# Kernel tuning notes

Measured on AMD Instinct MI355X. Metric: run time of the kernel, lower is better.

The kernel has to match this reference:

```python
import jax, jax.numpy as jnp
import numpy as np

E = 2048      # embed_dim
HQ = 16       # query heads
HK = 4        # kv heads
D = E // HQ   # head_dim = 128
G = HQ // HK  # head groups = 4
KVE = D * HK  # kv_embed_dim = 512
B, N = 2, 2048


def setup_inputs() -> dict:
    key = jax.random.key(0)
    ks = jax.random.split(key, 8)
    s_q = (2.0 / (E + E)) ** 0.5      # xavier_normal for square proj
    s_kv = (2.0 / (E + KVE)) ** 0.5   # xavier_normal for kv proj
    return {
        "query": jax.random.normal(ks[0], (B, N, E), jnp.float32),
        "key":   jax.random.normal(ks[1], (B, N, E), jnp.float32),
        "value": jax.random.normal(ks[2], (B, N, E), jnp.float32),
        "Wq": jax.random.normal(ks[3], (E, E), jnp.float32) * s_q,
        "bq_": jnp.zeros((E,), jnp.float32),
        "Wk": jax.random.normal(ks[4], (KVE, E), jnp.float32) * s_kv,
        "bk_": jnp.zeros((KVE,), jnp.float32),
        "Wv": jax.random.normal(ks[5], (KVE, E), jnp.float32) * s_kv,
        "bv_": jnp.zeros((KVE,), jnp.float32),
        "Wo": jax.random.normal(ks[6], (E, E), jnp.float32) * s_q,
        "bo_": jnp.zeros((E,), jnp.float32),
        "is_causal": 1,
    }


def reference(query, key, value, Wq, bq_, Wk, bk_, Wv, bv_, Wo, bo_, is_causal):
    b, n, _ = query.shape
    s = key.shape[1]
    # projections (torch Linear: y = x @ W.T + b)
    q = (query @ Wq.T + bq_).reshape(b, n, HQ, D).transpose(0, 2, 1, 3)  # b hq n d
    k = (key   @ Wk.T + bk_).reshape(b, s, HK, D).transpose(0, 2, 1, 3)  # b hk s d
    v = (value @ Wv.T + bv_).reshape(b, s, HK, D).transpose(0, 2, 1, 3)  # b hk s d
    q = q / (D ** 0.5)
    # split query heads 'b (h g) n d -> b g h n d' (h = kv heads outer, g inner)
    qg = q.reshape(b, HK, G, n, D).transpose(0, 2, 1, 3, 4)              # b g h n d
    sim = jnp.einsum('bghnd,bhsd->bghns', qg, k)                          # b g h n s
    if is_causal:
        causal = jnp.tril(jnp.ones((n, s), dtype=bool))
        sim = jnp.where(causal, sim, jnp.finfo(sim.dtype).min)
    attn = jax.nn.softmax(sim, axis=-1)
    out = jnp.einsum('bghns,bhsd->bghnd', attn, v)                        # b g h n d
    # 'b g h n d -> b n (h g) d' then merge heads
    out = out.transpose(0, 3, 2, 1, 4).reshape(b, n, E)
    return out @ Wo.T + bo_
```

## Files before the change

### kernel.cpp

```cpp
#include <hip/hip_runtime.h>
#include <stdint.h>

#define E_   2048
#define HQ_  16
#define HK_  4
#define D_   128
#define G_   4
#define KVE_ 512
#define B_   2
#define N_   2048
#define MTOT (B_*N_)

#define QSC 0.12751743f

typedef __attribute__((ext_vector_type(8))) short bf16x8;
typedef __attribute__((ext_vector_type(4))) float f32x4;

__device__ __forceinline__ unsigned short f2bf(float f) {
  union { float f; uint32_t u; } a; a.f = f;
  uint32_t u = a.u;
  uint32_t r = (u + 0x7fffu + ((u >> 16) & 1u)) >> 16;
  return (unsigned short)r;
}

__device__ __forceinline__ uint32_t pack_bf2(float a, float b) {
  union { float f; uint32_t u; } x, y; x.f = a; y.f = b;
  return (x.u >> 16) | (y.u & 0xffff0000u);
}

__device__ __forceinline__ void g2l16(const void* g, void* l) {
  __builtin_amdgcn_global_load_lds(
      (__attribute__((address_space(1))) void*)(void*)(uintptr_t)g,
      (__attribute__((address_space(3))) void*)l,
      16, 0, 0);
}

__global__ void cast_all(const float* __restrict__ q, const float* __restrict__ k,
                         const float* __restrict__ v, const float* __restrict__ wq,
                         const float* __restrict__ wk, const float* __restrict__ wv,
                         const float* __restrict__ wo, unsigned short* __restrict__ dst) {
  int i = blockIdx.x * 256 + threadIdx.x;
  const float* src; int base;
  if      (i < 2097152) { src = q;  base = 0; }
  else if (i < 4194304) { src = k;  base = 2097152; }
  else if (i < 6291456) { src = v;  base = 4194304; }
  else if (i < 7340032) { src = wq; base = 6291456; }
  else if (i < 7602176) { src = wk; base = 7340032; }
  else if (i < 7864320) { src = wv; base = 7602176; }
  else                  { src = wo; base = 7864320; }
  float4 val = ((const float4*)src)[i - base];
  ushort4 o;
  o.x = f2bf(val.x); o.y = f2bf(val.y); o.z = f2bf(val.z); o.w = f2bf(val.w);
  ((ushort4*)dst)[i] = o;
}

__device__ __forceinline__ void gemm_kloop(const unsigned short* __restrict__ A,
                                           const unsigned short* __restrict__ W,
                                           unsigned short* As, unsigned short* Bs,
                                           int bm, int bn, int K,
                                           int wm, int wn, int tid, int l16, int quad,
                                           f32x4 acc[4][4]) {
  for (int k0 = 0; k0 < K; k0 += 32) {
    __syncthreads();
#pragma unroll
    for (int r = 0; r < 2; ++r) {
      int c = r * 256 + tid;
      int row = c >> 2, c8 = (c & 3) << 3;
      g2l16(A + (size_t)(bm + row) * K + k0 + c8, (char*)As + (size_t)c * 16);
    }
#pragma unroll
    for (int r = 0; r < 2; ++r) {
      int c = r * 256 + tid;
      int row = c >> 2, c8 = (c & 3) << 3;
      g2l16(W + (size_t)(bn + row) * K + k0 + c8, (char*)Bs + (size_t)c * 16);
    }
    __syncthreads();

    bf16x8 af[4], bf[4];
#pragma unroll
    for (int mi = 0; mi < 4; ++mi)
      af[mi] = *(const bf16x8*)(As + (wm + mi * 16 + l16) * 32 + quad * 8);
#pragma unroll
    for (int ni = 0; ni < 4; ++ni)
      bf[ni] = *(const bf16x8*)(Bs + (wn + ni * 16 + l16) * 32 + quad * 8);
#pragma unroll
    for (int mi = 0; mi < 4; ++mi)
#pragma unroll
      for (int ni = 0; ni < 4; ++ni)
        acc[mi][ni] = __builtin_amdgcn_mfma_f32_16x16x32_bf16(af[mi], bf[ni], acc[mi][ni], 0, 0, 0);
  }
}

__global__ __launch_bounds__(256, 3)
void proj_fused(const unsigned short* __restrict__ qb, const unsigned short* __restrict__ kb,
                const unsigned short* __restrict__ vb,
                const unsigned short* __restrict__ Wqb, const unsigned short* __restrict__ Wkb,
                const unsigned short* __restrict__ Wvb,
                const float* __restrict__ bq, const float* __restrict__ bk,
                const float* __restrict__ bv,
                unsigned short* __restrict__ Qb, unsigned short* __restrict__ Kpp,
                unsigned short* __restrict__ Vtt) {
  __shared__ unsigned short As[128 * 32];
  __shared__ unsigned short Bs[128 * 32];
  const int tid  = threadIdx.x;
  const int wave = tid >> 6, lane = tid & 63;
  const int l16  = lane & 15, quad = lane >> 4;
  const int bm = blockIdx.x * 128;
  const int wm = (wave & 1) * 64, wn = (wave >> 1) * 64;
  const int y = blockIdx.y;

  const unsigned short *A, *W;
  const float* bias;
  unsigned short* out;
  int bn, mode, Nn;
  float scale;
  if (y < 16)      { A = qb; W = Wqb; bias = bq; out = Qb;  bn = y * 128;        mode = 0; Nn = 2048; scale = QSC;  }
  else if (y < 20) { A = kb; W = Wkb; bias = bk; out = Kpp; bn = (y - 16) * 128; mode = 0; Nn = 512;  scale = 1.0f; }
  else             { A = vb; W = Wvb; bias = bv; out = Vtt; bn = (y - 20) * 128; mode = 1; Nn = 512;  scale = 1.0f; }

  f32x4 acc[4][4] = {};
  gemm_kloop(A, W, As, Bs, bm, bn, E_, wm, wn, tid, l16, quad, acc);

  if (mode == 0) {
#pragma unroll
    for (int mi = 0; mi < 4; ++mi)
#pragma unroll
      for (int ni = 0; ni < 4; ++ni) {
        int col = bn + wn + ni * 16 + l16;
        float bb = bias[col];
        int row0 = bm + wm + mi * 16 + quad * 4;
#pragma unroll
        for (int r = 0; r < 4; ++r)
          out[(size_t)(row0 + r) * Nn + col] = f2bf((acc[mi][ni][r] + bb) * scale);
      }
  } else {
#pragma unroll
    for (int mi = 0; mi < 4; ++mi)
#pragma unroll
      for (int ni = 0; ni < 4; ++ni) {
        int col = bn + wn + ni * 16 + l16;
        float bb = bias[col];
        int row0 = bm + wm + mi * 16 + quad * 4;
        int b = row0 >> 11, s = row0 & 2047;
        ushort4 o;
        o.x = f2bf(acc[mi][ni][0] + bb);
        o.y = f2bf(acc[mi][ni][1] + bb);
        o.z = f2bf(acc[mi][ni][2] + bb);
        o.w = f2bf(acc[mi][ni][3] + bb);
        *(ushort4*)(out + (size_t)(b * KVE_ + col) * N_ + s) = o;
      }
  }
}

__global__ __launch_bounds__(256, 2)
void gemm_out(const unsigned short* __restrict__ A, const unsigned short* __restrict__ W,
              const float* __restrict__ bias, float* __restrict__ Cout) {
  __shared__ unsigned short As[128 * 32];
  __shared__ unsigned short Bs[128 * 32];
  const int tid  = threadIdx.x;
  const int wave = tid >> 6, lane = tid & 63;
  const int l16  = lane & 15, quad = lane >> 4;
  const int bm = blockIdx.x * 128, bn = blockIdx.y * 128;
  const int wm = (wave & 1) * 64, wn = (wave >> 1) * 64;

  f32x4 acc[4][4] = {};
  gemm_kloop(A, W, As, Bs, bm, bn, E_, wm, wn, tid, l16, quad, acc);

#pragma unroll
  for (int mi = 0; mi < 4; ++mi)
#pragma unroll
    for (int ni = 0; ni < 4; ++ni) {
      int col = bn + wn + ni * 16 + l16;
      float bb = bias[col];
      int row0 = bm + wm + mi * 16 + quad * 4;
#pragma unroll
      for (int r = 0; r < 4; ++r)
        Cout[(size_t)(row0 + r) * E_ + col] = acc[mi][ni][r] + bb;
    }
}

__global__ __launch_bounds__(256, 3)
void attn_gqa(const unsigned short* __restrict__ Qp,
              const unsigned short* __restrict__ Kp,
              const unsigned short* __restrict__ Vt,
              unsigned short* __restrict__ Ob,
              const int* __restrict__ is_causal_p) {
  __shared__ unsigned short lds[2][8192];
  __shared__ float Xt[256];

  const int tid  = threadIdx.x;
  const int wave = tid >> 6, lane = tid & 63;
  const int l16  = lane & 15, quad = lane >> 4;
  const int qg = wave >> 1, sg = wave & 1;
  const int bh = blockIdx.y;
  const int u  = (blockIdx.x + bh) & 31;
  const int qt = (u < 16) ? u : 47 - u;
  const int b = bh >> 4, hq = bh & 15, hk = hq >> 2;
  const int causal = *is_causal_p;

  const unsigned short* Kbase = Kp + (size_t)b * N_ * KVE_ + hk * D_;
  const unsigned short* Vbase = Vt + (size_t)(b * KVE_ + hk * D_) * N_;

  const int nt = causal ? qt + 1 : (N_ / 64);
  const int qw = qt * 64 + qg * 32;

  auto stage = [&](int t, int buf) {
    int s0 = t * 64;
    unsigned short* Kd = &lds[buf][0];
#pragma unroll
    for (int r = 0; r < 4; ++r) {
      int idx = r * 256 + tid;
      int s = (idx >> 8) * 16 + (idx & 15);
      int d = ((idx >> 6) & 3) * 32 + ((idx >> 4) & 3) * 8;
      g2l16(Kbase + (size_t)(s0 + s) * KVE_ + d, Kd + (size_t)idx * 8);
    }
  };

  bf16x8 qf[2][4];
#pragma unroll
  for (int mi = 0; mi < 2; ++mi)
#pragma unroll
    for (int kk = 0; kk < 4; ++kk)
      qf[mi][kk] = *(const bf16x8*)(Qp + (size_t)(b * N_ + qw + mi * 16 + l16) * E_ +
                                    hq * D_ + kk * 32 + quad * 8);

  f32x4 o[2][8] = {};
  float tsum[2] = { 0.f, 0.f };

  stage(0, 0);
  __syncthreads();

  for (int t = 0; t < nt; ++t) {
    if (t + 1 < nt) stage(t + 1, (t + 1) & 1);
    const unsigned short* Kb = &lds[t & 1][0];
    const int sw = t * 64 + sg * 32;
    const bool active = !causal || (sw <= qw + 31);

    if (active) {
      f32x4 sa[2][2] = {};
#pragma unroll
      for (int kk = 0; kk < 4; ++kk) {
        bf16x8 kf[2];
#pragma unroll
        for (int ni = 0; ni < 2; ++ni)
          kf[ni] = *(const bf16x8*)(Kb + (((sg * 2 + ni) * 4 + kk) * 64 + lane) * 8);
#pragma unroll
        for (int mi = 0; mi < 2; ++mi)
#pragma unroll
          for (int ni = 0; ni < 2; ++ni)
            sa[mi][ni] = __builtin_amdgcn_mfma_f32_16x16x32_bf16(kf[ni], qf[mi][kk], sa[mi][ni], 0, 0, 0);
      }

      bf16x8 vf[8];
#pragma unroll
      for (int n8 = 0; n8 < 8; ++n8)
        vf[n8] = *(const bf16x8*)(Vbase + (size_t)(n8 * 16 + l16) * N_ + sw + quad * 8);

      if (causal && sw + 31 > qw) {
#pragma unroll
        for (int mi = 0; mi < 2; ++mi)
#pragma unroll
          for (int ni = 0; ni < 2; ++ni) {
            int sbase = sw + ni * 16 + quad * 4;
            int q = qw + mi * 16 + l16;
#pragma unroll
            for (int r = 0; r < 4; ++r)
              if (sbase + r > q) sa[mi][ni][r] = -3.0e38f;
          }
      }

      uint32_t pk[2][2][2];
#pragma unroll
      for (int mi = 0; mi < 2; ++mi)
#pragma unroll
        for (int ni = 0; ni < 2; ++ni) {
#pragma unroll
          for (int r = 0; r < 4; ++r) {
            float e = __builtin_amdgcn_exp2f(sa[mi][ni][r]);
            tsum[mi] += e;
            sa[mi][ni][r] = e;
          }
          pk[mi][ni][0] = pack_bf2(sa[mi][ni][0], sa[mi][ni][1]);
          pk[mi][ni][1] = pack_bf2(sa[mi][ni][2], sa[mi][ni][3]);
        }

#pragma unroll
      for (int mi = 0; mi < 2; ++mi) {
        union { bf16x8 v; uint32_t w[4]; } pb;
#pragma unroll
        for (int h = 0; h < 4; ++h) {
          int src = ((quad & 1) * 2 + (h >> 1)) * 16 + l16;
          uint32_t v0 = __shfl(pk[mi][0][h & 1], src);
          uint32_t v1 = __shfl(pk[mi][1][h & 1], src);
          pb.w[h] = (quad & 2) ? v1 : v0;
        }
#pragma unroll
        for (int n8 = 0; n8 < 8; ++n8)
          o[mi][n8] = __builtin_amdgcn_mfma_f32_16x16x32_bf16(vf[n8], pb.v, o[mi][n8], 0, 0, 0);
      }
    }
    __syncthreads();
  }

  float4* X4 = (float4*)&lds[0][0];
  if (sg == 1) {
#pragma unroll
    for (int mi = 0; mi < 2; ++mi) {
#pragma unroll
      for (int ni = 0; ni < 8; ++ni) {
        float4 w;
        w.x = o[mi][ni][0]; w.y = o[mi][ni][1]; w.z = o[mi][ni][2]; w.w = o[mi][ni][3];
        X4[((qg * 2 + mi) * 8 + ni) * 64 + lane] = w;
      }
      Xt[(qg * 2 + mi) * 64 + lane] = tsum[mi];
    }
  }
  __syncthreads();
  if (sg == 0) {
#pragma unroll
    for (int mi = 0; mi < 2; ++mi) {
      float lt = tsum[mi] + Xt[(qg * 2 + mi) * 64 + lane];
      lt += __shfl_xor(lt, 16);
      lt += __shfl_xor(lt, 32);
      float inv = 1.0f / lt;
      int q = qw + mi * 16 + l16;
#pragma unroll
      for (int ni = 0; ni < 8; ++ni) {
        float4 xx = X4[((qg * 2 + mi) * 8 + ni) * 64 + lane];
        ushort4 st;
        st.x = f2bf((o[mi][ni][0] + xx.x) * inv);
        st.y = f2bf((o[mi][ni][1] + xx.y) * inv);
        st.z = f2bf((o[mi][ni][2] + xx.z) * inv);
        st.w = f2bf((o[mi][ni][3] + xx.w) * inv);
        *(ushort4*)(Ob + (size_t)(b * N_ + q) * E_ + hq * D_ + ni * 16 + quad * 4) = st;
      }
    }
  }
}

extern "C" void kernel_launch(void* const* d_in, const int* in_sizes, int n_in,
                              void* d_out, int out_size, void* d_ws, size_t ws_size,
                              hipStream_t stream) {
  const float* query = (const float*)d_in[0];
  const float* key   = (const float*)d_in[1];
  const float* value = (const float*)d_in[2];
  const float* Wq = (const float*)d_in[3];
  const float* bq = (const float*)d_in[4];
  const float* Wk = (const float*)d_in[5];
  const float* bk = (const float*)d_in[6];
  const float* Wv = (const float*)d_in[7];
  const float* bv = (const float*)d_in[8];
  const float* Wo = (const float*)d_in[9];
  const float* bo = (const float*)d_in[10];
  const int* is_causal = (const int*)d_in[11];

  char* ws = (char*)d_ws;
  size_t off = 0;
  auto alloc = [&](size_t bytes) {
    char* p = ws + off;
    off += (bytes + 255) & ~(size_t)255;
    return p;
  };
  unsigned short* qb  = (unsigned short*)alloc((size_t)MTOT * E_ * 2);
  unsigned short* kb  = (unsigned short*)alloc((size_t)MTOT * E_ * 2);
  unsigned short* vb  = (unsigned short*)alloc((size_t)MTOT * E_ * 2);
  unsigned short* Wqb = (unsigned short*)alloc((size_t)E_ * E_ * 2);
  unsigned short* Wkb = (unsigned short*)alloc((size_t)KVE_ * E_ * 2);
  unsigned short* Wvb = (unsigned short*)alloc((size_t)KVE_ * E_ * 2);
  unsigned short* Wob = (unsigned short*)alloc((size_t)E_ * E_ * 2);
  unsigned short* Qb  = (unsigned short*)alloc((size_t)MTOT * E_ * 2);
  unsigned short* Kpp = (unsigned short*)alloc((size_t)MTOT * KVE_ * 2);
  unsigned short* Vtt = (unsigned short*)alloc((size_t)MTOT * KVE_ * 2);
  unsigned short* Ob  = (unsigned short*)alloc((size_t)MTOT * E_ * 2);
  (void)ws_size; (void)n_in; (void)in_sizes; (void)out_size;

  dim3 blk(256);
  cast_all<<<dim3(34816), blk, 0, stream>>>(query, key, value, Wq, Wk, Wv, Wo, qb);
  proj_fused<<<dim3(32, 24), blk, 0, stream>>>(qb, kb, vb, Wqb, Wkb, Wvb,
                                               bq, bk, bv, Qb, Kpp, Vtt);
  attn_gqa<<<dim3(32, 32), blk, 0, stream>>>(Qb, Kpp, Vtt, Ob, is_causal);
  gemm_out<<<dim3(32, 16), blk, 0, stream>>>(Ob, Wob, bo, (float*)d_out);
}
```

Before: 437.2 us.

## Use swizzled 64-wide K tiles in GEMMs and stage V through LDS in attention

The shared GEMM k-loop now loads 64-wide K slices into LDS with an XOR swizzle, halving the number of barrier pairs and aiming to avoid LDS bank conflicts on fragment reads. The attention kernel now stages V tiles into a single LDS buffer alongside K, instead of reading V fragments straight from global memory, and adds a mid-iteration barrier so the next tile's prefetch can reuse that buffer. This doubles GEMM LDS use, which may lower occupancy. The extra barrier per attention iteration may serialise more.

```diff
diff --git a/kernel.cpp b/kernel.cpp
--- a/kernel.cpp
+++ b/kernel.cpp
@@ -60,34 +60,42 @@
                                            int bm, int bn, int K,
                                            int wm, int wn, int tid, int l16, int quad,
                                            f32x4 acc[4][4]) {
-  for (int k0 = 0; k0 < K; k0 += 32) {
+  const int swz = l16 & 7;
+  for (int k0 = 0; k0 < K; k0 += 64) {
     __syncthreads();
 #pragma unroll
-    for (int r = 0; r < 2; ++r) {
+    for (int r = 0; r < 4; ++r) {
       int c = r * 256 + tid;
-      int row = c >> 2, c8 = (c & 3) << 3;
-      g2l16(A + (size_t)(bm + row) * K + k0 + c8, (char*)As + (size_t)c * 16);
-    }
-#pragma unroll
-    for (int r = 0; r < 2; ++r) {
+      int row = c >> 3;
+      int gs = ((c & 7) ^ (row & 7)) << 3;
+      g2l16(A + (size_t)(bm + row) * K + k0 + gs, (char*)As + (size_t)c * 16);
+    }
+#pragma unroll
+    for (int r = 0; r < 4; ++r) {
       int c = r * 256 + tid;
-      int row = c >> 2, c8 = (c & 3) << 3;
-      g2l16(W + (size_t)(bn + row) * K + k0 + c8, (char*)Bs + (size_t)c * 16);
+      int row = c >> 3;
+      int gs = ((c & 7) ^ (row & 7)) << 3;
+      g2l16(W + (size_t)(bn + row) * K + k0 + gs, (char*)Bs + (size_t)c * 16);
     }
     __syncthreads();
 
-    bf16x8 af[4], bf[4];
-#pragma unroll
-    for (int mi = 0; mi < 4; ++mi)
-      af[mi] = *(const bf16x8*)(As + (wm + mi * 16 + l16) * 32 + quad * 8);
-#pragma unroll
-    for (int ni = 0; ni < 4; ++ni)
-      bf[ni] = *(const bf16x8*)(Bs + (wn + ni * 16 + l16) * 32 + quad * 8);
-#pragma unroll
-    for (int mi = 0; mi < 4; ++mi)
+#pragma unroll
+    for (int kk = 0; kk < 2; ++kk) {
+      bf16x8 af[4], bf[4];
+#pragma unroll
+      for (int mi = 0; mi < 4; ++mi)
+        af[mi] = *(const bf16x8*)(As + (size_t)(wm + mi * 16 + l16) * 64 +
+                                  ((((kk << 2) | quad) ^ swz) << 3));
 #pragma unroll
       for (int ni = 0; ni < 4; ++ni)
-        acc[mi][ni] = __builtin_amdgcn_mfma_f32_16x16x32_bf16(af[mi], bf[ni], acc[mi][ni], 0, 0, 0);
+        bf[ni] = *(const bf16x8*)(Bs + (size_t)(wn + ni * 16 + l16) * 64 +
+                                  ((((kk << 2) | quad) ^ swz) << 3));
+#pragma unroll
+      for (int mi = 0; mi < 4; ++mi)
+#pragma unroll
+        for (int ni = 0; ni < 4; ++ni)
+          acc[mi][ni] = __builtin_amdgcn_mfma_f32_16x16x32_bf16(af[mi], bf[ni], acc[mi][ni], 0, 0, 0);
+    }
   }
 }
 
@@ -100,8 +108,8 @@
                 const float* __restrict__ bv,
                 unsigned short* __restrict__ Qb, unsigned short* __restrict__ Kpp,
                 unsigned short* __restrict__ Vtt) {
-  __shared__ unsigned short As[128 * 32];
-  __shared__ unsigned short Bs[128 * 32];
+  __shared__ unsigned short As[128 * 64];
+  __shared__ unsigned short Bs[128 * 64];
   const int tid  = threadIdx.x;
   const int wave = tid >> 6, lane = tid & 63;
   const int l16  = lane & 15, quad = lane >> 4;
@@ -155,8 +163,8 @@
 __global__ __launch_bounds__(256, 2)
 void gemm_out(const unsigned short* __restrict__ A, const unsigned short* __restrict__ W,
               const float* __restrict__ bias, float* __restrict__ Cout) {
-  __shared__ unsigned short As[128 * 32];
-  __shared__ unsigned short Bs[128 * 32];
+  __shared__ unsigned short As[128 * 64];
+  __shared__ unsigned short Bs[128 * 64];
   const int tid  = threadIdx.x;
   const int wave = tid >> 6, lane = tid & 63;
   const int l16  = lane & 15, quad = lane >> 4;
@@ -185,7 +193,8 @@
               const unsigned short* __restrict__ Vt,
               unsigned short* __restrict__ Ob,
               const int* __restrict__ is_causal_p) {
-  __shared__ unsigned short lds[2][8192];
+  __shared__ unsigned short Klds[2][8192];
+  __shared__ unsigned short Vlds[8192];
   __shared__ float Xt[256];
 
   const int tid  = threadIdx.x;
@@ -204,9 +213,9 @@
   const int nt = causal ? qt + 1 : (N_ / 64);
   const int qw = qt * 64 + qg * 32;
 
-  auto stage = [&](int t, int buf) {
+  auto stageK = [&](int t, int buf) {
     int s0 = t * 64;
-    unsigned short* Kd = &lds[buf][0];
+    unsigned short* Kd = &Klds[buf][0];
 #pragma unroll
     for (int r = 0; r < 4; ++r) {
       int idx = r * 256 + tid;
@@ -215,6 +224,16 @@
       g2l16(Kbase + (size_t)(s0 + s) * KVE_ + d, Kd + (size_t)idx * 8);
     }
   };
+  auto stageV = [&](int t) {
+    int s0 = t * 64;
+#pragma unroll
+    for (int r = 0; r < 4; ++r) {
+      int idx = r * 256 + tid;
+      int d = (idx >> 7) * 16 + (idx & 15);
+      int sc = ((idx >> 6) & 1) * 32 + ((idx >> 4) & 3) * 8;
+      g2l16(Vbase + (size_t)d * N_ + s0 + sc, Vlds + (size_t)idx * 8);
+    }
+  };
 
   bf16x8 qf[2][4];
 #pragma unroll
@@ -227,15 +246,17 @@
   f32x4 o[2][8] = {};
   float tsum[2] = { 0.f, 0.f };
 
-  stage(0, 0);
+  stageK(0, 0);
+  stageV(0);
   __syncthreads();
 
   for (int t = 0; t < nt; ++t) {
-    if (t + 1 < nt) stage(t + 1, (t + 1) & 1);
-    const unsigned short* Kb = &lds[t & 1][0];
+    const unsigned short* Kb = &Klds[t & 1][0];
     const int sw = t * 64 + sg * 32;
     const bool active = !causal || (sw <= qw + 31);
 
+    uint32_t pk[2][2][2];
+    bf16x8 vf[8];
     if (active) {
       f32x4 sa[2][2] = {};
 #pragma unroll
@@ -250,11 +271,6 @@
           for (int ni = 0; ni < 2; ++ni)
             sa[mi][ni] = __builtin_amdgcn_mfma_f32_16x16x32_bf16(kf[ni], qf[mi][kk], sa[mi][ni], 0, 0, 0);
       }
-
-      bf16x8 vf[8];
-#pragma unroll
-      for (int n8 = 0; n8 < 8; ++n8)
-        vf[n8] = *(const bf16x8*)(Vbase + (size_t)(n8 * 16 + l16) * N_ + sw + quad * 8);
 
       if (causal && sw + 31 > qw) {
 #pragma unroll
@@ -269,7 +285,6 @@
           }
       }
 
-      uint32_t pk[2][2][2];
 #pragma unroll
       for (int mi = 0; mi < 2; ++mi)
 #pragma unroll
@@ -284,6 +299,20 @@
           pk[mi][ni][1] = pack_bf2(sa[mi][ni][2], sa[mi][ni][3]);
         }
 
+      __builtin_amdgcn_sched_barrier(0);
+#pragma unroll
+      for (int n8 = 0; n8 < 8; ++n8)
+        vf[n8] = *(const bf16x8*)(Vlds + ((n8 * 2 + sg) * 64 + lane) * 8);
+    }
+
+    __syncthreads();
+
+    if (t + 1 < nt) {
+      stageK(t + 1, (t + 1) & 1);
+      stageV(t + 1);
+    }
+
+    if (active) {
 #pragma unroll
       for (int mi = 0; mi < 2; ++mi) {
         union { bf16x8 v; uint32_t w[4]; } pb;
@@ -299,10 +328,11 @@
           o[mi][n8] = __builtin_amdgcn_mfma_f32_16x16x32_bf16(vf[n8], pb.v, o[mi][n8], 0, 0, 0);
       }
     }
+
     __syncthreads();
   }
 
-  float4* X4 = (float4*)&lds[0][0];
+  float4* X4 = (float4*)&Klds[0][0];
   if (sg == 1) {
 #pragma unroll
     for (int mi = 0; mi < 2; ++mi) {
```

After: 393.6 us. -10.0%, faster.
